# Optimization experiments

Hardware: AMD Instinct MI355X
Metric: run time of the kernel (lower is better)

The kernel has to match this reference:

```python
import jax, jax.numpy as jnp
import numpy as np
import math

B, C, H, W = 2, 512, 64, 64
NUM_HEADS = 8
D_K = C // NUM_HEADS
SCALE = 1.0 / math.sqrt(D_K)


def setup_inputs() -> dict:
    key = jax.random.key(0)
    ks = jax.random.split(key, 7)
    init = 0.02
    return {
        "x": jax.random.normal(ks[0], (B, C, H, W), dtype=jnp.float32),
        "Wq": jax.random.normal(ks[1], (C, C), dtype=jnp.float32) * init,
        "bq": jnp.zeros((C,), dtype=jnp.float32),
        "Wkv": jax.random.normal(ks[2], (2 * C, C), dtype=jnp.float32) * init,
        "bkv": jnp.zeros((2 * C,), dtype=jnp.float32),
        "Wp": jax.random.normal(ks[3], (C, C), dtype=jnp.float32) * init,
        "bp": jnp.zeros((C,), dtype=jnp.float32),
    }


def _conv1x1(x, w, b):
    # x: [b, c_in, h, w], w: [c_out, c_in] (1x1 conv kernel), b: [c_out]
    return jnp.einsum('bchw,oc->bohw', x, w) + b[None, :, None, None]


def reference(x, Wq, bq, Wkv, bkv, Wp, bp):
    b, c, h, w = x.shape
    l = h * w
    q = _conv1x1(x, Wq, bq)
    kv = _conv1x1(x, Wkv, bkv)
    k, v = jnp.split(kv, 2, axis=1)
    # reshape to [b, heads, d_k, l]
    q = q.reshape(b, NUM_HEADS, D_K, l)
    k = k.reshape(b, NUM_HEADS, D_K, l)
    v = v.reshape(b, NUM_HEADS, D_K, l)
    attn = jnp.einsum('bhct,bhcs->bhts', q, k) * SCALE  # [b,h,l,l]
    attn = jax.nn.softmax(attn, axis=-1)
    out = jnp.einsum('bhts,bhcs->bhct', attn, v)  # [b,h,d_k,l]
    out = out.reshape(b, c, h, w)
    out = _conv1x1(out, Wp, bp)
    return out
```

## Files before the change

### kernel.cpp

```cpp
#include <hip/hip_runtime.h>
#include <math.h>

#define L_SEQ 4096
#define C_DIM 512
#define NH 8
#define DK 64
#define NB 2
#define QSC 0.18033688011112042f

typedef _Float16 f16;
typedef _Float16 f16x8 __attribute__((ext_vector_type(8)));
typedef _Float16 f16x4 __attribute__((ext_vector_type(4)));
typedef __fp16 h16x2 __attribute__((ext_vector_type(2)));
typedef float f32x4 __attribute__((ext_vector_type(4)));
typedef float f32x16 __attribute__((ext_vector_type(16)));
typedef unsigned int u32;

__global__ __launch_bounds__(256) void prep(
    const float* __restrict__ X, const float* __restrict__ Wq,
    const float* __restrict__ Wkv, const float* __restrict__ Wp,
    f16* __restrict__ Xt, f16* __restrict__ Wqkh,
    f16* __restrict__ Wvh, f16* __restrict__ Wph)
{
    const int tid = threadIdx.x;
    const int z = blockIdx.z;
    if (z < 2) {
        __shared__ f16 Ts[64][72];
        const float* src = X + (size_t)z * C_DIM * L_SEQ;
        f16* dst = Xt + (size_t)z * L_SEQ * C_DIM;
        for (int tile = blockIdx.x; tile < 512; tile += gridDim.x) {
            const int c0 = (tile & 7) * 64;
            const int t0 = (tile >> 3) * 64;
            __syncthreads();
            #pragma unroll
            for (int p = 0; p < 4; ++p) {
                const int c = (tid >> 4) + p * 16;
                const int t = (tid & 15) * 4;
                const float4 v = *(const float4*)(src + (size_t)(c0 + c) * L_SEQ + t0 + t);
                Ts[t + 0][c] = (f16)v.x; Ts[t + 1][c] = (f16)v.y;
                Ts[t + 2][c] = (f16)v.z; Ts[t + 3][c] = (f16)v.w;
            }
            __syncthreads();
            #pragma unroll
            for (int p = 0; p < 2; ++p) {
                const int t = (tid >> 3) + p * 32;
                const int ch = (tid & 7) * 8;
                *(f16x8*)(dst + (size_t)(t0 + t) * C_DIM + c0 + ch) =
                    *(const f16x8*)&Ts[t][ch];
            }
        }
    } else {
        const float* srcs[4] = {Wq, Wkv, Wkv + 262144, Wp};
        f16* dsts[4] = {Wqkh, Wqkh + 262144, Wvh, Wph};
        #pragma unroll
        for (int s = 0; s < 4; ++s) {
            const float* sp = srcs[s]; f16* dp = dsts[s];
            for (int i = blockIdx.x * 256 + tid; i < 65536; i += gridDim.x * 256) {
                const float4 v = *(const float4*)(sp + (size_t)i * 4);
                f16x4 h; h[0] = (f16)v.x; h[1] = (f16)v.y; h[2] = (f16)v.z; h[3] = (f16)v.w;
                *(f16x4*)(dp + (size_t)i * 4) = h;
            }
        }
    }
}

__global__ __launch_bounds__(256) void qk_mfma(
    const f16* __restrict__ Xt, const f16* __restrict__ Wqkh,
    const float* __restrict__ bq, const float* __restrict__ bkv,
    f16* __restrict__ Qh, f16* __restrict__ Kh)
{
    __shared__ f16 As[128][40];
    __shared__ f16 Bs[128][40];
    const int tid = threadIdx.x;
    const int lane = tid & 63, w = tid >> 6;
    const int l15 = lane & 15, quad = lane >> 4;
    const int wy = w >> 1, wx = w & 1;
    const int mb0 = blockIdx.x * 128;
    const int n0  = blockIdx.y * 128;

    f32x4 acc[4][4] = {};
    const int row = tid >> 2, c8 = (tid & 3) * 8;
    const f16* aptr = Xt + (size_t)mb0 * 512;
    const f16* bptr = Wqkh + (size_t)n0 * 512;

    uint4 ga0 = *(const uint4*)(aptr + (size_t)row * 512 + c8);
    uint4 ga1 = *(const uint4*)(aptr + (size_t)(row + 64) * 512 + c8);
    uint4 gb0 = *(const uint4*)(bptr + (size_t)row * 512 + c8);
    uint4 gb1 = *(const uint4*)(bptr + (size_t)(row + 64) * 512 + c8);

    for (int k0 = 0; k0 < 512; k0 += 32) {
        __syncthreads();
        *(uint4*)&As[row][c8] = ga0;
        *(uint4*)&As[row + 64][c8] = ga1;
        *(uint4*)&Bs[row][c8] = gb0;
        *(uint4*)&Bs[row + 64][c8] = gb1;
        if (k0 + 32 < 512) {
            ga0 = *(const uint4*)(aptr + (size_t)row * 512 + k0 + 32 + c8);
            ga1 = *(const uint4*)(aptr + (size_t)(row + 64) * 512 + k0 + 32 + c8);
            gb0 = *(const uint4*)(bptr + (size_t)row * 512 + k0 + 32 + c8);
            gb1 = *(const uint4*)(bptr + (size_t)(row + 64) * 512 + k0 + 32 + c8);
        }
        __syncthreads();
        f16x8 af[4], bf[4];
        #pragma unroll
        for (int i = 0; i < 4; ++i)
            af[i] = *(const f16x8*)&As[wy * 64 + i * 16 + l15][quad * 8];
        #pragma unroll
        for (int n = 0; n < 4; ++n)
            bf[n] = *(const f16x8*)&Bs[wx * 64 + n * 16 + l15][quad * 8];
        #pragma unroll
        for (int i = 0; i < 4; ++i)
            #pragma unroll
            for (int n = 0; n < 4; ++n)
                acc[i][n] = __builtin_amdgcn_mfma_f32_16x16x32_f16(af[i], bf[n], acc[i][n], 0, 0, 0);
    }

    #pragma unroll
    for (int nn = 0; nn < 4; ++nn) {
        const int o = n0 + wx * 64 + nn * 16 + l15;
        const bool isQ = (o < 512);
        const float bias = isQ ? bq[o] : bkv[o - 512];
        const int h = (o & 511) >> 6, d = o & 63;
        f16* base = isQ ? Qh : Kh;
        #pragma unroll
        for (int i = 0; i < 4; ++i) {
            const int tr = mb0 + wy * 64 + i * 16 + quad * 4;
            #pragma unroll
            for (int r = 0; r < 4; ++r) {
                const int tg = tr + r;
                const int bh = (tg >> 12) * NH + h;
                float v = acc[i][nn][r] + bias;
                if (isQ) v *= QSC;
                base[((size_t)bh * L_SEQ + (tg & 4095)) * DK + d] = (f16)v;
            }
        }
    }
}

__global__ __launch_bounds__(256) void cproj_mfma(
    const f16* __restrict__ Bsrc, const f16* __restrict__ Wh,
    const float* __restrict__ bias, f16* __restrict__ outV,
    float* __restrict__ outP, int mode)
{
    __shared__ f16 As[128][40];
    __shared__ f16 Bs[128][40];
    const int tid = threadIdx.x;
    const int lane = tid & 63, w = tid >> 6;
    const int l15 = lane & 15, quad = lane >> 4;
    const int wy = w >> 1, wx = w & 1;
    const int n0  = blockIdx.x * 128;
    const int mb0 = blockIdx.y * 128;

    f32x4 acc[4][4] = {};
    const int row = tid >> 2, c8 = (tid & 3) * 8;
    const f16* aptr = Wh + (size_t)mb0 * 512;
    const f16* bptr = Bsrc + (size_t)n0 * 512;

    uint4 ga0 = *(const uint4*)(aptr + (size_t)row * 512 + c8);
    uint4 ga1 = *(const uint4*)(aptr + (size_t)(row + 64) * 512 + c8);
    uint4 gb0 = *(const uint4*)(bptr + (size_t)row * 512 + c8);
    uint4 gb1 = *(const uint4*)(bptr + (size_t)(row + 64) * 512 + c8);

    for (int k0 = 0; k0 < 512; k0 += 32) {
        __syncthreads();
        *(uint4*)&As[row][c8] = ga0;
        *(uint4*)&As[row + 64][c8] = ga1;
        *(uint4*)&Bs[row][c8] = gb0;
        *(uint4*)&Bs[row + 64][c8] = gb1;
        if (k0 + 32 < 512) {
            ga0 = *(const uint4*)(aptr + (size_t)row * 512 + k0 + 32 + c8);
            ga1 = *(const uint4*)(aptr + (size_t)(row + 64) * 512 + k0 + 32 + c8);
            gb0 = *(const uint4*)(bptr + (size_t)row * 512 + k0 + 32 + c8);
            gb1 = *(const uint4*)(bptr + (size_t)(row + 64) * 512 + k0 + 32 + c8);
        }
        __syncthreads();
        f16x8 af[4], bf[4];
        #pragma unroll
        for (int i = 0; i < 4; ++i)
            af[i] = *(const f16x8*)&As[wy * 64 + i * 16 + l15][quad * 8];
        #pragma unroll
        for (int n = 0; n < 4; ++n)
            bf[n] = *(const f16x8*)&Bs[wx * 64 + n * 16 + l15][quad * 8];
        #pragma unroll
        for (int i = 0; i < 4; ++i)
            #pragma unroll
            for (int n = 0; n < 4; ++n)
                acc[i][n] = __builtin_amdgcn_mfma_f32_16x16x32_f16(af[i], bf[n], acc[i][n], 0, 0, 0);
    }

    const int l15p = (l15 & 3) | ((l15 & 4) << 1) | ((l15 & 8) >> 1);

    #pragma unroll
    for (int i = 0; i < 4; ++i) {
        #pragma unroll
        for (int r = 0; r < 4; ++r) {
            const int o = mb0 + wy * 64 + i * 16 + quad * 4 + r;
            const float bv = bias[o];
            #pragma unroll
            for (int nn = 0; nn < 4; ++nn) {
                const int tg = n0 + wx * 64 + nn * 16 + l15;
                const float v = acc[i][nn][r] + bv;
                if (mode == 0) {
                    const int tgp = (tg & ~15) | l15p;
                    const int bh = (tgp >> 12) * NH + (o >> 6);
                    outV[((size_t)bh * DK + (o & 63)) * L_SEQ + (tgp & 4095)] = (f16)v;
                } else {
                    outP[((size_t)(tg >> 12) * C_DIM + o) * L_SEQ + (tg & 4095)] = v;
                }
            }
        }
    }
}

__device__ __forceinline__ void gload_lds16(const char* g, char* l) {
    __builtin_amdgcn_global_load_lds(
        (const __attribute__((address_space(1))) void*)g,
        (__attribute__((address_space(3))) void*)l, 16, 0, 0);
}

__global__ __launch_bounds__(256, 4) void flash16(
    const f16* __restrict__ Qh, const f16* __restrict__ Kh,
    const f16* __restrict__ Vh, f16* __restrict__ Opart,
    float* __restrict__ Lpart)
{
    __shared__ f16 KS[2][64 * 64];
    __shared__ f16 VS[2][64 * 64];
    const int tid = threadIdx.x;
    const int lane = tid & 63, w = tid >> 6;
    const int l31 = lane & 31, hl = lane >> 5;
    const int bh = blockIdx.x;
    const int t0 = blockIdx.y * 128;
    const int half = blockIdx.z;
    const int s_beg = half * 2048, s_end = s_beg + 2048;
    const int wtb = t0 + w * 32;
    const f16* Qg = Qh + (size_t)bh * L_SEQ * DK;
    const char* Kg = (const char*)(Kh + (size_t)bh * L_SEQ * DK);
    const char* Vg = (const char*)(Vh + (size_t)bh * DK * L_SEQ);

    f16x8 qf[4];
    #pragma unroll
    for (int kst = 0; kst < 4; ++kst)
        qf[kst] = *(const f16x8*)(Qg + (size_t)(wtb + l31) * DK + kst * 16 + hl * 8);

    const int c0 = tid, c1 = tid + 256;
    const int kofs0 = (c0 >> 3) * 128  + (((c0 & 7) * 16) ^ (((c0 >> 3) & 7) << 4));
    const int kofs1 = (c1 >> 3) * 128  + (((c1 & 7) * 16) ^ (((c1 >> 3) & 7) << 4));
    const int vofs0 = (c0 >> 3) * 8192 + (((c0 & 7) * 16) ^ (((c0 >> 3) & 7) << 4));
    const int vofs1 = (c1 >> 3) * 8192 + (((c1 & 7) * 16) ^ (((c1 >> 3) & 7) << 4));
    const int lb0 = (w * 64) * 16, lb1 = (256 + w * 64) * 16;

    #define STAGE(bufi, s0v) do {                                   \
        const char* kg_ = Kg + (size_t)(s0v) * 128;                 \
        const char* vg_ = Vg + (size_t)(s0v) * 2;                   \
        char* kl_ = (char*)&KS[bufi][0];                            \
        char* vl_ = (char*)&VS[bufi][0];                            \
        gload_lds16(kg_ + kofs0, kl_ + lb0);                        \
        gload_lds16(kg_ + kofs1, kl_ + lb1);                        \
        gload_lds16(vg_ + vofs0, vl_ + lb0);                        \
        gload_lds16(vg_ + vofs1, vl_ + lb1);                        \
    } while (0)

    f32x16 O0 = {}, O1 = {};
    float rs = 0.f;
    h16x2 one2; one2[0] = (__fp16)1.f; one2[1] = (__fp16)1.f;

    STAGE(0, s_beg);
    __syncthreads();

    const int swz = (l31 & 7) << 4;
    const int rowA = l31 * 128, rowB = (32 + l31) * 128;

    int cur = 0;
    for (int s0 = s_beg; s0 < s_end; s0 += 64) {
        if (s0 + 64 < s_end) STAGE(cur ^ 1, s0 + 64);

        const char* Kb = (const char*)&KS[cur][0];
        const char* Vb = (const char*)&VS[cur][0];

        f32x16 S0 = {}, S1 = {};
        __builtin_amdgcn_s_setprio(1);
        #pragma unroll
        for (int kst = 0; kst < 4; ++kst) {
            const int cb = (kst * 32 + hl * 16) ^ swz;
            const f16x8 k0 = *(const f16x8*)(Kb + rowA + cb);
            const f16x8 k1 = *(const f16x8*)(Kb + rowB + cb);
            S0 = __builtin_amdgcn_mfma_f32_32x32x16_f16(k0, qf[kst], S0, 0, 0, 0);
            S1 = __builtin_amdgcn_mfma_f32_32x32x16_f16(k1, qf[kst], S1, 0, 0, 0);
        }
        __builtin_amdgcn_s_setprio(0);

        union FR { u32 u[4]; f16x8 v; } fr[4];
        #pragma unroll
        for (int q = 0; q < 4; ++q) {
            const h16x2 a01 = __builtin_amdgcn_cvt_pkrtz(
                __builtin_amdgcn_exp2f(S0[4 * q + 0]),
                __builtin_amdgcn_exp2f(S0[4 * q + 1]));
            const h16x2 a23 = __builtin_amdgcn_cvt_pkrtz(
                __builtin_amdgcn_exp2f(S0[4 * q + 2]),
                __builtin_amdgcn_exp2f(S0[4 * q + 3]));
            rs = __builtin_amdgcn_fdot2(a01, one2, rs, false);
            rs = __builtin_amdgcn_fdot2(a23, one2, rs, false);
            union { h16x2 h; u32 u; } p0, p1; p0.h = a01; p1.h = a23;
            fr[q >> 1].u[(q & 1) * 2 + 0] = p0.u;
            fr[q >> 1].u[(q & 1) * 2 + 1] = p1.u;
        }
        #pragma unroll
        for (int q = 0; q < 4; ++q) {
            const h16x2 a01 = __builtin_amdgcn_cvt_pkrtz(
                __builtin_amdgcn_exp2f(S1[4 * q + 0]),
                __builtin_amdgcn_exp2f(S1[4 * q + 1]));
            const h16x2 a23 = __builtin_amdgcn_cvt_pkrtz(
                __builtin_amdgcn_exp2f(S1[4 * q + 2]),
                __builtin_amdgcn_exp2f(S1[4 * q + 3]));
            rs = __builtin_amdgcn_fdot2(a01, one2, rs, false);
            rs = __builtin_amdgcn_fdot2(a23, one2, rs, false);
            union { h16x2 h; u32 u; } p0, p1; p0.h = a01; p1.h = a23;
            fr[2 + (q >> 1)].u[(q & 1) * 2 + 0] = p0.u;
            fr[2 + (q >> 1)].u[(q & 1) * 2 + 1] = p1.u;
        }

        __builtin_amdgcn_s_setprio(1);
        #pragma unroll
        for (int kst = 0; kst < 4; ++kst) {
            const int ca = (kst * 32 + hl * 16) ^ swz;
            const f16x8 v0 = *(const f16x8*)(Vb + rowA + ca);
            const f16x8 v1 = *(const f16x8*)(Vb + rowB + ca);
            O0 = __builtin_amdgcn_mfma_f32_32x32x16_f16(v0, fr[kst].v, O0, 0, 0, 0);
            O1 = __builtin_amdgcn_mfma_f32_32x32x16_f16(v1, fr[kst].v, O1, 0, 0, 0);
        }
        __builtin_amdgcn_s_setprio(0);

        __syncthreads();
        cur ^= 1;
    }
    #undef STAGE

    rs += __shfl_xor(rs, 32, 64);
    if (lane < 32)
        Lpart[(size_t)(half * 16 + bh) * L_SEQ + wtb + l31] = rs;

    f16* Op = Opart + (size_t)(half * 16 + bh) * DK * L_SEQ;
    #pragma unroll
    for (int r = 0; r < 16; ++r) {
        const int d = (r & 3) + 8 * (r >> 2) + 4 * hl;
        Op[(size_t)d * L_SEQ + wtb + l31] = (f16)O0[r];
        Op[(size_t)(32 + d) * L_SEQ + wtb + l31] = (f16)O1[r];
    }
}

__global__ __launch_bounds__(256) void combine(
    const f16* __restrict__ Opart, const float* __restrict__ Lpart,
    f16* __restrict__ Oh)
{
    __shared__ f16 Ts[64][72];
    __shared__ float Linv[64];
    const int tid = threadIdx.x;
    const int bh = blockIdx.y, b = bh >> 3, h = bh & 7;
    const int t0 = blockIdx.x * 64;
    if (tid < 64) {
        const float lo = Lpart[(size_t)bh * L_SEQ + t0 + tid];
        const float hi = Lpart[(size_t)(16 + bh) * L_SEQ + t0 + tid];
        Linv[tid] = 1.f / (lo + hi);
    }
    __syncthreads();
    const f16* Plo = Opart + (size_t)bh * DK * L_SEQ;
    const f16* Phi = Opart + (size_t)(16 + bh) * DK * L_SEQ;
    const int d = tid >> 4;
    const int tt = (tid & 15) * 4;
    #pragma unroll
    for (int p = 0; p < 4; ++p) {
        const int dd = d + p * 16;
        const size_t off = (size_t)dd * L_SEQ + t0 + tt;
        const f16x4 lo = *(const f16x4*)(Plo + off);
        const f16x4 hi = *(const f16x4*)(Phi + off);
        #pragma unroll
        for (int j = 0; j < 4; ++j)
            Ts[tt + j][dd] = (f16)(((float)lo[j] + (float)hi[j]) * Linv[tt + j]);
    }
    __syncthreads();
    const int tr = tid >> 2, ch = (tid & 3) * 16;
    f16* dst = Oh + ((size_t)(b * L_SEQ + t0 + tr)) * C_DIM + h * DK + ch;
    *(f16x8*)dst = *(const f16x8*)&Ts[tr][ch];
    *(f16x8*)(dst + 8) = *(const f16x8*)&Ts[tr][ch + 8];
}

extern "C" void kernel_launch(void* const* d_in, const int* in_sizes, int n_in,
                              void* d_out, int out_size, void* d_ws, size_t ws_size,
                              hipStream_t stream) {
    (void)in_sizes; (void)n_in; (void)out_size; (void)ws_size;
    const float* x   = (const float*)d_in[0];
    const float* Wq  = (const float*)d_in[1];
    const float* bq  = (const float*)d_in[2];
    const float* Wkv = (const float*)d_in[3];
    const float* bkv = (const float*)d_in[4];
    const float* Wp  = (const float*)d_in[5];
    const float* bp  = (const float*)d_in[6];
    float* out = (float*)d_out;

    f16* Xt    = (f16*)d_ws;
    f16* Wqkh  = Xt + 4194304;
    f16* Wvh   = Wqkh + 524288;
    f16* Wph   = Wvh + 262144;
    f16* Qh    = Wph + 262144;
    f16* Kh    = Qh + 4194304;
    f16* Vh    = Kh + 4194304;
    f16* Oh    = Vh + 4194304;
    f16* Opart = Oh + 4194304;
    float* Lpart = (float*)(Opart + 8388608);

    prep<<<dim3(128, 1, 3), 256, 0, stream>>>(x, Wq, Wkv, Wp, Xt, Wqkh, Wvh, Wph);
    qk_mfma<<<dim3(64, 8), 256, 0, stream>>>(Xt, Wqkh, bq, bkv, Qh, Kh);
    cproj_mfma<<<dim3(64, 4), 256, 0, stream>>>(Xt, Wvh, bkv + 512, Vh, nullptr, 0);
    flash16<<<dim3(16, 32, 2), 256, 0, stream>>>(Qh, Kh, Vh, Opart, Lpart);
    combine<<<dim3(64, 16), 256, 0, stream>>>(Opart, Lpart, Oh);
    cproj_mfma<<<dim3(64, 4), 256, 0, stream>>>(Oh, Wph, bp, nullptr, out, 1);
}
```

Measured before the change: 213.6 us.

## Process 64 query rows per wave in flash kernel to reuse K/V fragments

Each wave now handles two 32-row query tiles instead of one, so every K and V fragment read from LDS feeds two MFMAs. The block covers 256 query rows, which halves the grid along the query axis and halves total K/V global-to-LDS staging traffic. In exchange register pressure roughly doubles (four S and four O accumulators), launch bounds drop to 2 blocks per CU, and there are half as many blocks (512) to spread across the CUs.

```diff
diff --git a/kernel.cpp b/kernel.cpp
--- a/kernel.cpp
+++ b/kernel.cpp
@@ -218,7 +218,7 @@
         (__attribute__((address_space(3))) void*)l, 16, 0, 0);
 }
 
-__global__ __launch_bounds__(256, 4) void flash16(
+__global__ __launch_bounds__(256, 2) void flash16(
     const f16* __restrict__ Qh, const f16* __restrict__ Kh,
     const f16* __restrict__ Vh, f16* __restrict__ Opart,
     float* __restrict__ Lpart)
@@ -229,18 +229,20 @@
     const int lane = tid & 63, w = tid >> 6;
     const int l31 = lane & 31, hl = lane >> 5;
     const int bh = blockIdx.x;
-    const int t0 = blockIdx.y * 128;
+    const int t0 = blockIdx.y * 256;
     const int half = blockIdx.z;
     const int s_beg = half * 2048, s_end = s_beg + 2048;
-    const int wtb = t0 + w * 32;
+    const int wtb = t0 + w * 64;
     const f16* Qg = Qh + (size_t)bh * L_SEQ * DK;
     const char* Kg = (const char*)(Kh + (size_t)bh * L_SEQ * DK);
     const char* Vg = (const char*)(Vh + (size_t)bh * DK * L_SEQ);
 
-    f16x8 qf[4];
+    f16x8 qf0[4], qf1[4];
     #pragma unroll
-    for (int kst = 0; kst < 4; ++kst)
-        qf[kst] = *(const f16x8*)(Qg + (size_t)(wtb + l31) * DK + kst * 16 + hl * 8);
+    for (int kst = 0; kst < 4; ++kst) {
+        qf0[kst] = *(const f16x8*)(Qg + (size_t)(wtb + l31) * DK + kst * 16 + hl * 8);
+        qf1[kst] = *(const f16x8*)(Qg + (size_t)(wtb + 32 + l31) * DK + kst * 16 + hl * 8);
+    }
 
     const int c0 = tid, c1 = tid + 256;
     const int kofs0 = (c0 >> 3) * 128  + (((c0 & 7) * 16) ^ (((c0 >> 3) & 7) << 4));
@@ -260,8 +262,8 @@
         gload_lds16(vg_ + vofs1, vl_ + lb1);                        \
     } while (0)
 
-    f32x16 O0 = {}, O1 = {};
-    float rs = 0.f;
+    f32x16 O00 = {}, O01 = {}, O10 = {}, O11 = {};
+    float rs0 = 0.f, rs1 = 0.f;
     h16x2 one2; one2[0] = (__fp16)1.f; one2[1] = (__fp16)1.f;
 
     STAGE(0, s_beg);
@@ -277,46 +279,76 @@
         const char* Kb = (const char*)&KS[cur][0];
         const char* Vb = (const char*)&VS[cur][0];
 
-        f32x16 S0 = {}, S1 = {};
+        f32x16 Sa0 = {}, Sa1 = {}, Sb0 = {}, Sb1 = {};
         __builtin_amdgcn_s_setprio(1);
         #pragma unroll
         for (int kst = 0; kst < 4; ++kst) {
             const int cb = (kst * 32 + hl * 16) ^ swz;
             const f16x8 k0 = *(const f16x8*)(Kb + rowA + cb);
             const f16x8 k1 = *(const f16x8*)(Kb + rowB + cb);
-            S0 = __builtin_amdgcn_mfma_f32_32x32x16_f16(k0, qf[kst], S0, 0, 0, 0);
-            S1 = __builtin_amdgcn_mfma_f32_32x32x16_f16(k1, qf[kst], S1, 0, 0, 0);
+            Sa0 = __builtin_amdgcn_mfma_f32_32x32x16_f16(k0, qf0[kst], Sa0, 0, 0, 0);
+            Sa1 = __builtin_amdgcn_mfma_f32_32x32x16_f16(k0, qf1[kst], Sa1, 0, 0, 0);
+            Sb0 = __builtin_amdgcn_mfma_f32_32x32x16_f16(k1, qf0[kst], Sb0, 0, 0, 0);
+            Sb1 = __builtin_amdgcn_mfma_f32_32x32x16_f16(k1, qf1[kst], Sb1, 0, 0, 0);
         }
         __builtin_amdgcn_s_setprio(0);
 
-        union FR { u32 u[4]; f16x8 v; } fr[4];
+        union FR { u32 u[4]; f16x8 v; } fr0[4], fr1[4];
         #pragma unroll
         for (int q = 0; q < 4; ++q) {
             const h16x2 a01 = __builtin_amdgcn_cvt_pkrtz(
-                __builtin_amdgcn_exp2f(S0[4 * q + 0]),
-                __builtin_amdgcn_exp2f(S0[4 * q + 1]));
+                __builtin_amdgcn_exp2f(Sa0[4 * q + 0]),
+                __builtin_amdgcn_exp2f(Sa0[4 * q + 1]));
             const h16x2 a23 = __builtin_amdgcn_cvt_pkrtz(
-                __builtin_amdgcn_exp2f(S0[4 * q + 2]),
-                __builtin_amdgcn_exp2f(S0[4 * q + 3]));
-            rs = __builtin_amdgcn_fdot2(a01, one2, rs, false);
-            rs = __builtin_amdgcn_fdot2(a23, one2, rs, false);
+                __builtin_amdgcn_exp2f(Sa0[4 * q + 2]),
+                __builtin_amdgcn_exp2f(Sa0[4 * q + 3]));
+            rs0 = __builtin_amdgcn_fdot2(a01, one2, rs0, false);
+            rs0 = __builtin_amdgcn_fdot2(a23, one2, rs0, false);
             union { h16x2 h; u32 u; } p0, p1; p0.h = a01; p1.h = a23;
-            fr[q >> 1].u[(q & 1) * 2 + 0] = p0.u;
-            fr[q >> 1].u[(q & 1) * 2 + 1] = p1.u;
+            fr0[q >> 1].u[(q & 1) * 2 + 0] = p0.u;
+            fr0[q >> 1].u[(q & 1) * 2 + 1] = p1.u;
         }
         #pragma unroll
         for (int q = 0; q < 4; ++q) {
             const h16x2 a01 = __builtin_amdgcn_cvt_pkrtz(
-                __builtin_amdgcn_exp2f(S1[4 * q + 0]),
-                __builtin_amdgcn_exp2f(S1[4 * q + 1]));
+                __builtin_amdgcn_exp2f(Sb0[4 * q + 0]),
+                __builtin_amdgcn_exp2f(Sb0[4 * q + 1]));
             const h16x2 a23 = __builtin_amdgcn_cvt_pkrtz(
-                __builtin_amdgcn_exp2f(S1[4 * q + 2]),
-                __builtin_amdgcn_exp2f(S1[4 * q + 3]));
-            rs = __builtin_amdgcn_fdot2(a01, one2, rs, false);
-            rs = __builtin_amdgcn_fdot2(a23, one2, rs, false);
+                __builtin_amdgcn_exp2f(Sb0[4 * q + 2]),
+                __builtin_amdgcn_exp2f(Sb0[4 * q + 3]));
+            rs0 = __builtin_amdgcn_fdot2(a01, one2, rs0, false);
+            rs0 = __builtin_amdgcn_fdot2(a23, one2, rs0, false);
             union { h16x2 h; u32 u; } p0, p1; p0.h = a01; p1.h = a23;
-            fr[2 + (q >> 1)].u[(q & 1) * 2 + 0] = p0.u;
-            fr[2 + (q >> 1)].u[(q & 1) * 2 + 1] = p1.u;
+            fr0[2 + (q >> 1)].u[(q & 1) * 2 + 0] = p0.u;
+            fr0[2 + (q >> 1)].u[(q & 1) * 2 + 1] = p1.u;
+        }
+        #pragma unroll
+        for (int q = 0; q < 4; ++q) {
+            const h16x2 a01 = __builtin_amdgcn_cvt_pkrtz(
+                __builtin_amdgcn_exp2f(Sa1[4 * q + 0]),
+                __builtin_amdgcn_exp2f(Sa1[4 * q + 1]));
+            const h16x2 a23 = __builtin_amdgcn_cvt_pkrtz(
+                __builtin_amdgcn_exp2f(Sa1[4 * q + 2]),
+                __builtin_amdgcn_exp2f(Sa1[4 * q + 3]));
+            rs1 = __builtin_amdgcn_fdot2(a01, one2, rs1, false);
+            rs1 = __builtin_amdgcn_fdot2(a23, one2, rs1, false);
+            union { h16x2 h; u32 u; } p0, p1; p0.h = a01; p1.h = a23;
+            fr1[q >> 1].u[(q & 1) * 2 + 0] = p0.u;
+            fr1[q >> 1].u[(q & 1) * 2 + 1] = p1.u;
+        }
+        #pragma unroll
+        for (int q = 0; q < 4; ++q) {
+            const h16x2 a01 = __builtin_amdgcn_cvt_pkrtz(
+                __builtin_amdgcn_exp2f(Sb1[4 * q + 0]),
+                __builtin_amdgcn_exp2f(Sb1[4 * q + 1]));
+            const h16x2 a23 = __builtin_amdgcn_cvt_pkrtz(
+                __builtin_amdgcn_exp2f(Sb1[4 * q + 2]),
+                __builtin_amdgcn_exp2f(Sb1[4 * q + 3]));
+            rs1 = __builtin_amdgcn_fdot2(a01, one2, rs1, false);
+            rs1 = __builtin_amdgcn_fdot2(a23, one2, rs1, false);
+            union { h16x2 h; u32 u; } p0, p1; p0.h = a01; p1.h = a23;
+            fr1[2 + (q >> 1)].u[(q & 1) * 2 + 0] = p0.u;
+            fr1[2 + (q >> 1)].u[(q & 1) * 2 + 1] = p1.u;
         }
 
         __builtin_amdgcn_s_setprio(1);
@@ -325,8 +357,10 @@
             const int ca = (kst * 32 + hl * 16) ^ swz;
             const f16x8 v0 = *(const f16x8*)(Vb + rowA + ca);
             const f16x8 v1 = *(const f16x8*)(Vb + rowB + ca);
-            O0 = __builtin_amdgcn_mfma_f32_32x32x16_f16(v0, fr[kst].v, O0, 0, 0, 0);
-            O1 = __builtin_amdgcn_mfma_f32_32x32x16_f16(v1, fr[kst].v, O1, 0, 0, 0);
+            O00 = __builtin_amdgcn_mfma_f32_32x32x16_f16(v0, fr0[kst].v, O00, 0, 0, 0);
+            O01 = __builtin_amdgcn_mfma_f32_32x32x16_f16(v0, fr1[kst].v, O01, 0, 0, 0);
+            O10 = __builtin_amdgcn_mfma_f32_32x32x16_f16(v1, fr0[kst].v, O10, 0, 0, 0);
+            O11 = __builtin_amdgcn_mfma_f32_32x32x16_f16(v1, fr1[kst].v, O11, 0, 0, 0);
         }
         __builtin_amdgcn_s_setprio(0);
 
@@ -335,16 +369,22 @@
     }
     #undef STAGE
 
-    rs += __shfl_xor(rs, 32, 64);
-    if (lane < 32)
-        Lpart[(size_t)(half * 16 + bh) * L_SEQ + wtb + l31] = rs;
+    rs0 += __shfl_xor(rs0, 32, 64);
+    rs1 += __shfl_xor(rs1, 32, 64);
+    if (lane < 32) {
+        float* Lp = Lpart + (size_t)(half * 16 + bh) * L_SEQ + wtb;
+        Lp[l31] = rs0;
+        Lp[32 + l31] = rs1;
+    }
 
     f16* Op = Opart + (size_t)(half * 16 + bh) * DK * L_SEQ;
     #pragma unroll
     for (int r = 0; r < 16; ++r) {
         const int d = (r & 3) + 8 * (r >> 2) + 4 * hl;
-        Op[(size_t)d * L_SEQ + wtb + l31] = (f16)O0[r];
-        Op[(size_t)(32 + d) * L_SEQ + wtb + l31] = (f16)O1[r];
+        Op[(size_t)d * L_SEQ + wtb + l31] = (f16)O00[r];
+        Op[(size_t)d * L_SEQ + wtb + 32 + l31] = (f16)O01[r];
+        Op[(size_t)(32 + d) * L_SEQ + wtb + l31] = (f16)O10[r];
+        Op[(size_t)(32 + d) * L_SEQ + wtb + 32 + l31] = (f16)O11[r];
     }
 }
 
@@ -411,7 +451,7 @@
     prep<<<dim3(128, 1, 3), 256, 0, stream>>>(x, Wq, Wkv, Wp, Xt, Wqkh, Wvh, Wph);
     qk_mfma<<<dim3(64, 8), 256, 0, stream>>>(Xt, Wqkh, bq, bkv, Qh, Kh);
     cproj_mfma<<<dim3(64, 4), 256, 0, stream>>>(Xt, Wvh, bkv + 512, Vh, nullptr, 0);
-    flash16<<<dim3(16, 32, 2), 256, 0, stream>>>(Qh, Kh, Vh, Opart, Lpart);
+    flash16<<<dim3(16, 16, 2), 256, 0, stream>>>(Qh, Kh, Vh, Opart, Lpart);
     combine<<<dim3(64, 16), 256, 0, stream>>>(Opart, Lpart, Oh);
     cproj_mfma<<<dim3(64, 4), 256, 0, stream>>>(Oh, Wph, bp, nullptr, out, 1);
 }
```

Result: faster. 205.3 us (-3.9%).
